# Performance work log

Measured on AMD Instinct MI355X. Metric: run time of the kernel, lower is better.

The kernel has to match this reference:

```python
import jax, jax.numpy as jnp
import numpy as np

EMBED_DIM = 1024
NUM_HEADS = 16
HEAD_DIM = EMBED_DIM // NUM_HEADS
B, S = 4, 2048


def setup_inputs() -> dict:
    key = jax.random.key(0)
    ks = jax.random.split(key, 11)
    lim = 1.0 / np.sqrt(EMBED_DIM)
    def lin(k, out_dim, in_dim):
        return jax.random.uniform(k, (out_dim, in_dim), jnp.float32, -lim, lim)
    return {
        "query": jax.random.normal(ks[0], (B, S, EMBED_DIM), jnp.float32),
        "Wq": lin(ks[1], EMBED_DIM, EMBED_DIM), "bq": jnp.zeros((EMBED_DIM,), jnp.float32),
        "Wk": lin(ks[2], EMBED_DIM, EMBED_DIM), "bk": jnp.zeros((EMBED_DIM,), jnp.float32),
        "Wv": lin(ks[3], EMBED_DIM, EMBED_DIM), "bv": jnp.zeros((EMBED_DIM,), jnp.float32),
        "Wo": lin(ks[4], EMBED_DIM, EMBED_DIM), "bo": jnp.zeros((EMBED_DIM,), jnp.float32),
        "Wb": lin(ks[5], NUM_HEADS, EMBED_DIM), "bb": jnp.zeros((NUM_HEADS,), jnp.float32),
    }


def reference(query, Wq, bq, Wk, bk, Wv, bv, Wo, bo, Wb, bb):
    b, s, e = query.shape
    h, d = NUM_HEADS, HEAD_DIM
    scale = 1.0 / np.sqrt(d).astype(np.float32)
    # per-(batch, head) beta gate from mean-pooled query
    pooled = jnp.mean(query, axis=1)                       # [B, E]
    betas = jax.nn.sigmoid(pooled @ Wb.T + bb)             # [B, H]
    betas = betas[:, :, None, None]                        # [B, H, 1, 1]
    Q = (query @ Wq.T + bq).reshape(b, s, h, d).transpose(0, 2, 1, 3)
    K = (query @ Wk.T + bk).reshape(b, s, h, d).transpose(0, 2, 1, 3)
    V = (query @ Wv.T + bv).reshape(b, s, h, d).transpose(0, 2, 1, 3)
    scores = jnp.einsum('bhqd,bhkd->bhqk', Q, K) * scale   # [B, H, S, S]
    attn = jax.nn.softmax(scores * betas, axis=-1)
    out = jnp.einsum('bhqk,bhkd->bhqd', attn, V)           # [B, H, S, D]
    out = out.transpose(0, 2, 1, 3).reshape(b, s, e)
    return out @ Wo.T + bo
```

## Files before the change

kernel.cpp:

```cpp
#include <hip/hip_runtime.h>
#include <hip/hip_bf16.h>


typedef __bf16 bf16x8 __attribute__((ext_vector_type(8)));
typedef float f32x4 __attribute__((ext_vector_type(4)));
typedef unsigned short us4 __attribute__((ext_vector_type(4)));
typedef unsigned short us8 __attribute__((ext_vector_type(8)));
typedef unsigned int u32x4 __attribute__((ext_vector_type(4)));

#define LOG2E 1.4426950408889634f

static __device__ __forceinline__ void gl_lds16(const __bf16* g, __bf16* l) {
  __builtin_amdgcn_global_load_lds(
      (const __attribute__((address_space(1))) unsigned int*)g,
      (__attribute__((address_space(3))) unsigned int*)l, 16, 0, 0);
}

static __device__ __forceinline__ unsigned int cvtpk(float lo, float hi) {
  unsigned int r;
  asm("v_cvt_pk_bf16_f32 %0, %1, %2" : "=v"(r) : "v"(lo), "v"(hi));
  return r;
}

static __device__ __forceinline__ float exp2r(float x) {
#if __has_builtin(__builtin_amdgcn_exp2f)
  return __builtin_amdgcn_exp2f(x);
#else
  float r;
  asm("v_exp_f32 %0, %1" : "=v"(r) : "v"(x));
  return r;
#endif
}

__global__ __launch_bounds__(256) void pooled_cast(const float* __restrict__ q,
                                                   float* __restrict__ pooled,
                                                   __bf16* __restrict__ Xbf) {
  const int b = blockIdx.x >> 6;
  const int sc = (blockIdx.x >> 2) & 15;
  const int ec = blockIdx.x & 3;
  const int e = ec * 256 + threadIdx.x;
  const size_t base = (size_t)b * 2048 * 1024 + (size_t)sc * 128 * 1024 + e;
  const float* p = q + base;
  __bf16* xo = Xbf + base;
  float s = 0.f;
  for (int i = 0; i < 128; i++) {
    const float v = p[(size_t)i * 1024];
    s += v;
    xo[(size_t)i * 1024] = (__bf16)v;
  }
  atomicAdd(&pooled[b * 1024 + e], s * (1.0f / 2048.0f));
}

__global__ __launch_bounds__(256) void cast_w(const float* __restrict__ Wq,
                                              const float* __restrict__ Wk,
                                              const float* __restrict__ Wv,
                                              const float* __restrict__ Wo,
                                              __bf16* __restrict__ Wqkv,
                                              __bf16* __restrict__ Wob) {
  const int which = blockIdx.x >> 10;
  const int off = blockIdx.x & 1023;
  const float* src;
  __bf16* dst;
  if (which == 0) { src = Wq; dst = Wqkv; }
  else if (which == 1) { src = Wk; dst = Wqkv + 1024 * 1024; }
  else if (which == 2) { src = Wv; dst = Wqkv + 2 * 1024 * 1024; }
  else { src = Wo; dst = Wob; }
  const int i = off * 256 + threadIdx.x;
  const f32x4 v = *(const f32x4*)(src + (size_t)i * 4);
  us4 o;
#pragma unroll
  for (int j = 0; j < 4; j++) o[j] = __builtin_bit_cast(unsigned short, (__bf16)v[j]);
  *(us4*)(dst + (size_t)i * 4) = o;
}

__global__ __launch_bounds__(256) void betas_k(const float* __restrict__ pooled,
                                               const float* __restrict__ Wb,
                                               const float* __restrict__ bb,
                                               float* __restrict__ betas) {
  const int w = threadIdx.x >> 6, l = threadIdx.x & 63;
  const int idx = blockIdx.x * 4 + w;
  const int b = idx >> 4, h = idx & 15;
  float s = 0.f;
  for (int e = l; e < 1024; e += 64) s += pooled[b * 1024 + e] * Wb[h * 1024 + e];
#pragma unroll
  for (int m = 32; m >= 1; m >>= 1) s += __shfl_xor(s, m);
  if (l == 0) betas[idx] = 1.0f / (1.0f + __expf(-(s + bb[h])));
}

template <int EPI>
__global__ __launch_bounds__(256) void gemm_bt(
    const __bf16* __restrict__ A, const __bf16* __restrict__ Bm,
    const float* __restrict__ b0, const float* __restrict__ b1,
    const float* __restrict__ b2, const float* __restrict__ bet,
    __bf16* __restrict__ o0, __bf16* __restrict__ o1, __bf16* __restrict__ o2,
    float* __restrict__ of, const int M, const int N, const int K) {
  __shared__ __bf16 As[128 * 32];
  __shared__ __bf16 Bs[128 * 32];
  const int t = threadIdx.x;
  const int l = t & 63;
  const int w = t >> 6;
  const int wrow = w >> 1, wcol = w & 1;
  const int lr = l & 15, lq = l >> 4;
  const int blockM = blockIdx.y * 128;
  const int blockN = blockIdx.x * 128;
  const __bf16* Ab = A + (size_t)blockM * K;
  const __bf16* Bb = Bm + (size_t)blockN * K;
  const int srow = t >> 2;
  const int scol = (t & 3) * 8;

  f32x4 acc[4][4] = {};

  for (int kt = 0; kt < K; kt += 32) {
    gl_lds16(Ab + (size_t)srow * K + kt + scol, As + t * 8);
    gl_lds16(Ab + (size_t)(srow + 64) * K + kt + scol, As + 2048 + t * 8);
    gl_lds16(Bb + (size_t)srow * K + kt + scol, Bs + t * 8);
    gl_lds16(Bb + (size_t)(srow + 64) * K + kt + scol, Bs + 2048 + t * 8);
    __syncthreads();
    bf16x8 af[4], bf_[4];
#pragma unroll
    for (int i = 0; i < 4; i++)
      af[i] = *(const bf16x8*)&As[(wrow * 64 + i * 16 + lr) * 32 + lq * 8];
#pragma unroll
    for (int i = 0; i < 4; i++)
      bf_[i] = *(const bf16x8*)&Bs[(wcol * 64 + i * 16 + lr) * 32 + lq * 8];
#pragma unroll
    for (int i = 0; i < 4; i++)
#pragma unroll
      for (int j = 0; j < 4; j++)
        acc[i][j] = __builtin_amdgcn_mfma_f32_16x16x32_bf16(af[i], bf_[j], acc[i][j], 0, 0, 0);
    __syncthreads();
  }

  const int row0 = blockM + wrow * 64 + lq * 4;
  const int col0 = blockN + wcol * 64 + lr;
  if (EPI == 0) {
    const int which = blockN >> 10;
    const int b_ = blockM >> 11;
    const float* bias = (which == 0) ? b0 : ((which == 1) ? b1 : b2);
#pragma unroll
    for (int i = 0; i < 4; i++) {
#pragma unroll
      for (int j = 0; j < 4; j++) {
        const int col = col0 + j * 16;
        const int e = col & 1023;
        const int h = e >> 6, d = e & 63;
        const float bv = bias[e];
        if (which == 0) {
          const float qs = bet[b_ * 16 + h] * (0.125f * LOG2E);
#pragma unroll
          for (int jj = 0; jj < 4; jj++) {
            const int row = row0 + i * 16 + jj;
            o0[((size_t)(b_ * 16 + h) * 2048 + (row & 2047)) * 64 + d] =
                (__bf16)((acc[i][j][jj] + bv) * qs);
          }
        } else if (which == 1) {
#pragma unroll
          for (int jj = 0; jj < 4; jj++) {
            const int row = row0 + i * 16 + jj;
            o1[((size_t)(b_ * 16 + h) * 2048 + (row & 2047)) * 64 + d] =
                (__bf16)(acc[i][j][jj] + bv);
          }
        } else {
          const int s0 = (row0 + i * 16) & 2047;
          us4 pk;
#pragma unroll
          for (int jj = 0; jj < 4; jj++)
            pk[jj] = __builtin_bit_cast(unsigned short, (__bf16)(acc[i][j][jj] + bv));
          *(us4*)&o2[((size_t)(b_ * 16 + h) * 64 + d) * 2048 + s0] = pk;
        }
      }
    }
  } else {
#pragma unroll
    for (int i = 0; i < 4; i++) {
#pragma unroll
      for (int j = 0; j < 4; j++) {
        const int col = col0 + j * 16;
        const float bv = b0[col];
#pragma unroll
        for (int jj = 0; jj < 4; jj++) {
          const int row = row0 + i * 16 + jj;
          of[(size_t)row * N + col] = acc[i][j][jj] + bv;
        }
      }
    }
  }
}

__global__ __launch_bounds__(256) void attn_fwd(const __bf16* __restrict__ Q,
                                                const __bf16* __restrict__ Kb,
                                                const __bf16* __restrict__ Vt,
                                                __bf16* __restrict__ AO) {
  __shared__ float smO[2][64][36];
  __shared__ float smD[4][64];

  const int t = threadIdx.x;
  const int w = t >> 6, l = t & 63;
  const int lr = l & 15, lq = l >> 4;
  const int bh = blockIdx.x >> 5;
  const int qb = blockIdx.x & 31;
  const int b = bh >> 4, h = bh & 15;

  const __bf16* Qp = Q + (size_t)bh * (2048 * 64) + (size_t)qb * (64 * 64);
  const __bf16* Kp = Kb + (size_t)bh * (2048 * 64);
  const __bf16* Vp = Vt + (size_t)bh * (64 * 2048);

  bf16x8 aq[4][2];
#pragma unroll
  for (int qf = 0; qf < 4; qf++)
#pragma unroll
    for (int kc = 0; kc < 2; kc++)
      aq[qf][kc] = *(const bf16x8*)&Qp[(qf * 16 + lr) * 64 + kc * 32 + lq * 8];

  f32x4 o[4][4] = {};
  float dAcc[4] = {0.f, 0.f, 0.f, 0.f};

  for (int tile = w; tile < 64; tile += 4) {
    const int kbase = tile * 32;
    bf16x8 vfr[4];
#pragma unroll
    for (int df = 0; df < 4; df++)
      vfr[df] = *(const bf16x8*)&Vp[(size_t)(df * 16 + lr) * 2048 + kbase + lq * 8];
    bf16x8 kfr[2][2];
#pragma unroll
    for (int kf = 0; kf < 2; kf++)
#pragma unroll
      for (int kc = 0; kc < 2; kc++)
        kfr[kf][kc] = *(const bf16x8*)&Kp[(size_t)(kbase + kf * 16 + lr) * 64 + kc * 32 + lq * 8];

#pragma unroll
    for (int qf = 0; qf < 4; qf++) {
      f32x4 st0 = {}, st1 = {};
      st0 = __builtin_amdgcn_mfma_f32_16x16x32_bf16(kfr[0][0], aq[qf][0], st0, 0, 0, 0);
      st0 = __builtin_amdgcn_mfma_f32_16x16x32_bf16(kfr[0][1], aq[qf][1], st0, 0, 0, 0);
      st1 = __builtin_amdgcn_mfma_f32_16x16x32_bf16(kfr[1][0], aq[qf][0], st1, 0, 0, 0);
      st1 = __builtin_amdgcn_mfma_f32_16x16x32_bf16(kfr[1][1], aq[qf][1], st1, 0, 0, 0);
      float p0[4], p1[4];
#pragma unroll
      for (int jj = 0; jj < 4; jj++) p0[jj] = exp2r(st0[jj]);
#pragma unroll
      for (int jj = 0; jj < 4; jj++) p1[jj] = exp2r(st1[jj]);
      dAcc[qf] += ((p0[0] + p0[1]) + (p0[2] + p0[3])) + ((p1[0] + p1[1]) + (p1[2] + p1[3]));
      unsigned int x0 = cvtpk(p0[0], p0[1]), x1 = cvtpk(p0[2], p0[3]);
      unsigned int y0 = cvtpk(p1[0], p1[1]), y1 = cvtpk(p1[2], p1[3]);
      asm("v_permlane32_swap_b32 %0, %1" : "+v"(x0), "+v"(y0));
      asm("v_permlane16_swap_b32 %0, %1" : "+v"(x0), "+v"(y0));
      asm("v_permlane32_swap_b32 %0, %1" : "+v"(x1), "+v"(y1));
      asm("v_permlane16_swap_b32 %0, %1" : "+v"(x1), "+v"(y1));
      u32x4 pw = {x0, x1, y0, y1};
      const bf16x8 pa = __builtin_bit_cast(bf16x8, pw);
#pragma unroll
      for (int df = 0; df < 4; df++)
        o[qf][df] = __builtin_amdgcn_mfma_f32_16x16x32_bf16(pa, vfr[df], o[qf][df], 0, 0, 0);
    }
  }

#pragma unroll
  for (int qf = 0; qf < 4; qf++) {
    float dv = dAcc[qf];
    dv += __shfl_xor(dv, 16);
    dv += __shfl_xor(dv, 32);
    if (lq == 0) smD[w][qf * 16 + lr] = dv;
  }

  const int q = t >> 2;
  const int c8 = (t & 3) * 8;
  __bf16* op = AO + (size_t)b * (2048 * 1024) + (size_t)(qb * 64 + q) * 1024 + h * 64;
  float inv;

  if (w >= 2) {
#pragma unroll
    for (int qf = 0; qf < 4; qf++)
#pragma unroll
      for (int df = 0; df < 2; df++)
#pragma unroll
        for (int jj = 0; jj < 4; jj++)
          smO[w - 2][qf * 16 + lq * 4 + jj][df * 16 + lr] = o[qf][df][jj];
  }
  __syncthreads();
  if (w < 2) {
#pragma unroll
    for (int qf = 0; qf < 4; qf++)
#pragma unroll
      for (int df = 0; df < 2; df++)
#pragma unroll
        for (int jj = 0; jj < 4; jj++)
          smO[w][qf * 16 + lq * 4 + jj][df * 16 + lr] += o[qf][df][jj];
  }
  inv = 1.0f / (smD[0][q] + smD[1][q] + smD[2][q] + smD[3][q]);
  __syncthreads();
  {
    const f32x4 a0 = *(const f32x4*)&smO[0][q][c8];
    const f32x4 a1 = *(const f32x4*)&smO[0][q][c8 + 4];
    const f32x4 b0v = *(const f32x4*)&smO[1][q][c8];
    const f32x4 b1v = *(const f32x4*)&smO[1][q][c8 + 4];
    us8 pk;
#pragma unroll
    for (int c = 0; c < 4; c++) {
      pk[c] = __builtin_bit_cast(unsigned short, (__bf16)((a0[c] + b0v[c]) * inv));
      pk[c + 4] = __builtin_bit_cast(unsigned short, (__bf16)((a1[c] + b1v[c]) * inv));
    }
    *(us8*)(op + c8) = pk;
  }
  __syncthreads();

  if (w >= 2) {
#pragma unroll
    for (int qf = 0; qf < 4; qf++)
#pragma unroll
      for (int df = 2; df < 4; df++)
#pragma unroll
        for (int jj = 0; jj < 4; jj++)
          smO[w - 2][qf * 16 + lq * 4 + jj][(df - 2) * 16 + lr] = o[qf][df][jj];
  }
  __syncthreads();
  if (w < 2) {
#pragma unroll
    for (int qf = 0; qf < 4; qf++)
#pragma unroll
      for (int df = 2; df < 4; df++)
#pragma unroll
        for (int jj = 0; jj < 4; jj++)
          smO[w][qf * 16 + lq * 4 + jj][(df - 2) * 16 + lr] += o[qf][df][jj];
  }
  __syncthreads();
  {
    const f32x4 a0 = *(const f32x4*)&smO[0][q][c8];
    const f32x4 a1 = *(const f32x4*)&smO[0][q][c8 + 4];
    const f32x4 b0v = *(const f32x4*)&smO[1][q][c8];
    const f32x4 b1v = *(const f32x4*)&smO[1][q][c8 + 4];
    us8 pk;
#pragma unroll
    for (int c = 0; c < 4; c++) {
      pk[c] = __builtin_bit_cast(unsigned short, (__bf16)((a0[c] + b0v[c]) * inv));
      pk[c + 4] = __builtin_bit_cast(unsigned short, (__bf16)((a1[c] + b1v[c]) * inv));
    }
    *(us8*)(op + 32 + c8) = pk;
  }
}

extern "C" void kernel_launch(void* const* d_in, const int* in_sizes, int n_in,
                              void* d_out, int out_size, void* d_ws, size_t ws_size,
                              hipStream_t stream) {
  const float* query = (const float*)d_in[0];
  const float* Wq = (const float*)d_in[1];
  const float* bq = (const float*)d_in[2];
  const float* Wk = (const float*)d_in[3];
  const float* bk = (const float*)d_in[4];
  const float* Wv = (const float*)d_in[5];
  const float* bv = (const float*)d_in[6];
  const float* Wo = (const float*)d_in[7];
  const float* bo = (const float*)d_in[8];
  const float* Wb = (const float*)d_in[9];
  const float* bb = (const float*)d_in[10];
  float* out = (float*)d_out;

  char* ws = (char*)d_ws;
  __bf16* Xbf = (__bf16*)(ws);
  __bf16* Wqkv = (__bf16*)(ws + 16777216);
  __bf16* Wob = (__bf16*)(ws + 23068672);
  __bf16* Qb = (__bf16*)(ws + 25165824);
  __bf16* Kbuf = (__bf16*)(ws + 41943040);
  __bf16* Vt = (__bf16*)(ws + 58720256);
  float* pooled = (float*)(ws + 79691776);
  float* betas = (float*)(ws + 79708160);
  __bf16* AO = Xbf;

  hipMemsetAsync(pooled, 0, 4096 * sizeof(float), stream);
  pooled_cast<<<256, 256, 0, stream>>>(query, pooled, Xbf);
  cast_w<<<4096, 256, 0, stream>>>(Wq, Wk, Wv, Wo, Wqkv, Wob);
  betas_k<<<16, 256, 0, stream>>>(pooled, Wb, bb, betas);
  gemm_bt<0><<<dim3(24, 64), 256, 0, stream>>>(Xbf, Wqkv, bq, bk, bv, betas,
                                               Qb, Kbuf, Vt, nullptr, 8192, 3072, 1024);
  attn_fwd<<<2048, 256, 0, stream>>>(Qb, Kbuf, Vt, AO);
  gemm_bt<1><<<dim3(8, 64), 256, 0, stream>>>(AO, Wob, bo, nullptr, nullptr, nullptr,
                                              nullptr, nullptr, nullptr, out, 8192, 1024, 1024);
}
```

Measured before the change: 361.8 us.

## Split attention warps across query halves and key halves; widen pooled_cast grid

The attention kernel now assigns each wave half the query rows and half the key tiles (2x2 split) instead of all 64 queries over a quarter of keys, halving per-wave accumulator registers and adding a launch_bounds occupancy hint of 4 blocks. The cross-wave reduction becomes a single pairwise sum through a smaller shared buffer. Each wave now loads K/V for twice as many tiles relative to its compute, raising per-FLOP global/L2 traffic in exchange for higher occupancy. Separately, pooled_cast uses twice as many blocks with half the rows each to expose more parallelism.

```diff
diff --git a/kernel.cpp b/kernel.cpp
--- a/kernel.cpp
+++ b/kernel.cpp
@@ -35,15 +35,15 @@
 __global__ __launch_bounds__(256) void pooled_cast(const float* __restrict__ q,
                                                    float* __restrict__ pooled,
                                                    __bf16* __restrict__ Xbf) {
-  const int b = blockIdx.x >> 6;
-  const int sc = (blockIdx.x >> 2) & 15;
+  const int b = blockIdx.x >> 7;
+  const int sc = (blockIdx.x >> 2) & 31;
   const int ec = blockIdx.x & 3;
   const int e = ec * 256 + threadIdx.x;
-  const size_t base = (size_t)b * 2048 * 1024 + (size_t)sc * 128 * 1024 + e;
+  const size_t base = (size_t)b * 2048 * 1024 + (size_t)sc * 64 * 1024 + e;
   const float* p = q + base;
   __bf16* xo = Xbf + base;
   float s = 0.f;
-  for (int i = 0; i < 128; i++) {
+  for (int i = 0; i < 64; i++) {
     const float v = p[(size_t)i * 1024];
     s += v;
     xo[(size_t)i * 1024] = (__bf16)v;
@@ -187,16 +187,18 @@
   }
 }
 
-__global__ __launch_bounds__(256) void attn_fwd(const __bf16* __restrict__ Q,
-                                                const __bf16* __restrict__ Kb,
-                                                const __bf16* __restrict__ Vt,
-                                                __bf16* __restrict__ AO) {
-  __shared__ float smO[2][64][36];
-  __shared__ float smD[4][64];
+__global__ __launch_bounds__(256, 4) void attn_fwd(const __bf16* __restrict__ Q,
+                                                   const __bf16* __restrict__ Kb,
+                                                   const __bf16* __restrict__ Vt,
+                                                   __bf16* __restrict__ AO) {
+  __shared__ float smO[64][36];
+  __shared__ float smD[4][32];
 
   const int t = threadIdx.x;
   const int w = t >> 6, l = t & 63;
   const int lr = l & 15, lq = l >> 4;
+  const int qh = w >> 1;
+  const int kh = w & 1;
   const int bh = blockIdx.x >> 5;
   const int qb = blockIdx.x & 31;
   const int b = bh >> 4, h = bh & 15;
@@ -205,17 +207,17 @@
   const __bf16* Kp = Kb + (size_t)bh * (2048 * 64);
   const __bf16* Vp = Vt + (size_t)bh * (64 * 2048);
 
-  bf16x8 aq[4][2];
-#pragma unroll
-  for (int qf = 0; qf < 4; qf++)
+  bf16x8 aq[2][2];
+#pragma unroll
+  for (int qf = 0; qf < 2; qf++)
 #pragma unroll
     for (int kc = 0; kc < 2; kc++)
-      aq[qf][kc] = *(const bf16x8*)&Qp[(qf * 16 + lr) * 64 + kc * 32 + lq * 8];
-
-  f32x4 o[4][4] = {};
-  float dAcc[4] = {0.f, 0.f, 0.f, 0.f};
-
-  for (int tile = w; tile < 64; tile += 4) {
+      aq[qf][kc] = *(const bf16x8*)&Qp[(qh * 32 + qf * 16 + lr) * 64 + kc * 32 + lq * 8];
+
+  f32x4 o[2][4] = {};
+  float dAcc[2] = {0.f, 0.f};
+
+  for (int tile = kh; tile < 64; tile += 2) {
     const int kbase = tile * 32;
     bf16x8 vfr[4];
 #pragma unroll
@@ -229,7 +231,7 @@
         kfr[kf][kc] = *(const bf16x8*)&Kp[(size_t)(kbase + kf * 16 + lr) * 64 + kc * 32 + lq * 8];
 
 #pragma unroll
-    for (int qf = 0; qf < 4; qf++) {
+    for (int qf = 0; qf < 2; qf++) {
       f32x4 st0 = {}, st1 = {};
       st0 = __builtin_amdgcn_mfma_f32_16x16x32_bf16(kfr[0][0], aq[qf][0], st0, 0, 0, 0);
       st0 = __builtin_amdgcn_mfma_f32_16x16x32_bf16(kfr[0][1], aq[qf][1], st0, 0, 0, 0);
@@ -256,7 +258,7 @@
   }
 
 #pragma unroll
-  for (int qf = 0; qf < 4; qf++) {
+  for (int qf = 0; qf < 2; qf++) {
     float dv = dAcc[qf];
     dv += __shfl_xor(dv, 16);
     dv += __shfl_xor(dv, 32);
@@ -266,74 +268,69 @@
   const int q = t >> 2;
   const int c8 = (t & 3) * 8;
   __bf16* op = AO + (size_t)b * (2048 * 1024) + (size_t)(qb * 64 + q) * 1024 + h * 64;
-  float inv;
-
-  if (w >= 2) {
-#pragma unroll
-    for (int qf = 0; qf < 4; qf++)
+
+  if (kh == 1) {
+#pragma unroll
+    for (int qf = 0; qf < 2; qf++)
 #pragma unroll
       for (int df = 0; df < 2; df++)
 #pragma unroll
         for (int jj = 0; jj < 4; jj++)
-          smO[w - 2][qf * 16 + lq * 4 + jj][df * 16 + lr] = o[qf][df][jj];
-  }
-  __syncthreads();
-  if (w < 2) {
-#pragma unroll
-    for (int qf = 0; qf < 4; qf++)
+          smO[qh * 32 + qf * 16 + lq * 4 + jj][df * 16 + lr] = o[qf][df][jj];
+  }
+  __syncthreads();
+  if (kh == 0) {
+#pragma unroll
+    for (int qf = 0; qf < 2; qf++)
 #pragma unroll
       for (int df = 0; df < 2; df++)
 #pragma unroll
         for (int jj = 0; jj < 4; jj++)
-          smO[w][qf * 16 + lq * 4 + jj][df * 16 + lr] += o[qf][df][jj];
-  }
-  inv = 1.0f / (smD[0][q] + smD[1][q] + smD[2][q] + smD[3][q]);
+          smO[qh * 32 + qf * 16 + lq * 4 + jj][df * 16 + lr] += o[qf][df][jj];
+  }
+  const float inv = 1.0f / (smD[(q >> 5) * 2][q & 31] + smD[(q >> 5) * 2 + 1][q & 31]);
   __syncthreads();
   {
-    const f32x4 a0 = *(const f32x4*)&smO[0][q][c8];
-    const f32x4 a1 = *(const f32x4*)&smO[0][q][c8 + 4];
-    const f32x4 b0v = *(const f32x4*)&smO[1][q][c8];
-    const f32x4 b1v = *(const f32x4*)&smO[1][q][c8 + 4];
+    const f32x4 a0 = *(const f32x4*)&smO[q][c8];
+    const f32x4 a1 = *(const f32x4*)&smO[q][c8 + 4];
     us8 pk;
 #pragma unroll
     for (int c = 0; c < 4; c++) {
-      pk[c] = __builtin_bit_cast(unsigned short, (__bf16)((a0[c] + b0v[c]) * inv));
-      pk[c + 4] = __builtin_bit_cast(unsigned short, (__bf16)((a1[c] + b1v[c]) * inv));
+      pk[c] = __builtin_bit_cast(unsigned short, (__bf16)(a0[c] * inv));
+      pk[c + 4] = __builtin_bit_cast(unsigned short, (__bf16)(a1[c] * inv));
     }
     *(us8*)(op + c8) = pk;
   }
   __syncthreads();
 
-  if (w >= 2) {
-#pragma unroll
-    for (int qf = 0; qf < 4; qf++)
+  if (kh == 1) {
+#pragma unroll
+    for (int qf = 0; qf < 2; qf++)
 #pragma unroll
       for (int df = 2; df < 4; df++)
 #pragma unroll
         for (int jj = 0; jj < 4; jj++)
-          smO[w - 2][qf * 16 + lq * 4 + jj][(df - 2) * 16 + lr] = o[qf][df][jj];
-  }
-  __syncthreads();
-  if (w < 2) {
-#pragma unroll
-    for (int qf = 0; qf < 4; qf++)
+          smO[qh * 32 + qf * 16 + lq * 4 + jj][(df - 2) * 16 + lr] = o[qf][df][jj];
+  }
+  __syncthreads();
+  if (kh == 0) {
+#pragma unroll
+    for (int qf = 0; qf < 2; qf++)
 #pragma unroll
       for (int df = 2; df < 4; df++)
 #pragma unroll
         for (int jj = 0; jj < 4; jj++)
-          smO[w][qf * 16 + lq * 4 + jj][(df - 2) * 16 + lr] += o[qf][df][jj];
+          smO[qh * 32 + qf * 16 + lq * 4 + jj][(df - 2) * 16 + lr] += o[qf][df][jj];
   }
   __syncthreads();
   {
-    const f32x4 a0 = *(const f32x4*)&smO[0][q][c8];
-    const f32x4 a1 = *(const f32x4*)&smO[0][q][c8 + 4];
-    const f32x4 b0v = *(const f32x4*)&smO[1][q][c8];
-    const f32x4 b1v = *(const f32x4*)&smO[1][q][c8 + 4];
+    const f32x4 a0 = *(const f32x4*)&smO[q][c8];
+    const f32x4 a1 = *(const f32x4*)&smO[q][c8 + 4];
     us8 pk;
 #pragma unroll
     for (int c = 0; c < 4; c++) {
-      pk[c] = __builtin_bit_cast(unsigned short, (__bf16)((a0[c] + b0v[c]) * inv));
-      pk[c + 4] = __builtin_bit_cast(unsigned short, (__bf16)((a1[c] + b1v[c]) * inv));
+      pk[c] = __builtin_bit_cast(unsigned short, (__bf16)(a0[c] * inv));
+      pk[c + 4] = __builtin_bit_cast(unsigned short, (__bf16)(a1[c] * inv));
     }
     *(us8*)(op + 32 + c8) = pk;
   }
@@ -367,7 +364,7 @@
   __bf16* AO = Xbf;
 
   hipMemsetAsync(pooled, 0, 4096 * sizeof(float), stream);
-  pooled_cast<<<256, 256, 0, stream>>>(query, pooled, Xbf);
+  pooled_cast<<<512, 256, 0, stream>>>(query, pooled, Xbf);
   cast_w<<<4096, 256, 0, stream>>>(Wq, Wk, Wv, Wo, Wqkv, Wob);
   betas_k<<<16, 256, 0, stream>>>(pooled, Wb, bb, betas);
   gemm_bt<0><<<dim3(24, 64), 256, 0, stream>>>(Xbf, Wqkv, bq, bk, bv, betas,
```

Result: slower. 452.9 us (+25.2%).
